# Performance work log

Measured on AMD Instinct MI355X. Metric: run time of the kernel, lower is better.

## Reference

```python
import jax, jax.numpy as jnp
import numpy as np

SR = 32000
N_FFT = 1024
HOP = 320
N_MELS = 128
PCEN_EPS = 1e-6
LN_EPS = 1e-6


def _hz_to_mel(f):
    return 2595.0 * np.log10(1.0 + f / 700.0)


def _mel_to_hz(m):
    return 700.0 * (10.0 ** (m / 2595.0) - 1.0)


def make_mel_fb():
    # HTK-scale triangular mel filterbank, [n_freqs, n_mels] (torchaudio default)
    n_freqs = N_FFT // 2 + 1
    mels = np.linspace(_hz_to_mel(0.0), _hz_to_mel(SR / 2.0), N_MELS + 2)
    f_pts = _mel_to_hz(mels)                       # [n_mels+2]
    all_freqs = np.linspace(0.0, SR / 2.0, n_freqs)
    f_diff = f_pts[1:] - f_pts[:-1]
    slopes = f_pts[None, :] - all_freqs[:, None]   # [n_freqs, n_mels+2]
    down = -slopes[:, :-2] / f_diff[:-1]
    up = slopes[:, 2:] / f_diff[1:]
    fb = np.maximum(0.0, np.minimum(down, up))
    return fb.astype(np.float32)


def setup_inputs() -> dict:
    key = jax.random.key(0)
    x = jax.random.normal(key, (16, 320000), dtype=jnp.float32)
    return {
        "x": x,
        "mel_fb": jnp.asarray(make_mel_fb()),
        "log_s": jnp.asarray(np.log(0.025), dtype=jnp.float32),
        "log_alpha": jnp.asarray(np.log(0.98), dtype=jnp.float32),
        "log_delta": jnp.asarray(np.log(2.0), dtype=jnp.float32),
        "log_r": jnp.asarray(np.log(0.5), dtype=jnp.float32),
    }


def reference(x, mel_fb, log_s, log_alpha, log_delta, log_r):
    B, T = x.shape
    pad = N_FFT // 2
    xp = jnp.pad(x, ((0, 0), (pad, pad)), mode="reflect")
    n_frames = 1 + (xp.shape[1] - N_FFT) // HOP           # = T//HOP + 1
    idx = jnp.arange(n_frames)[:, None] * HOP + jnp.arange(N_FFT)[None, :]
    frames = xp[:, idx]                                    # [B, F, N_FFT]
    # periodic Hann window (torch.hann_window default)
    win = 0.5 * (1.0 - jnp.cos(2.0 * jnp.pi * jnp.arange(N_FFT) / N_FFT))
    spec = jnp.fft.rfft(frames * win, axis=-1)             # [B, F, N_FFT//2+1]
    power = spec.real ** 2 + spec.imag ** 2                # power spectrogram
    E = jnp.einsum("bfk,km->bfm", power, mel_fb)           # [B, F, M] mel energies

    s = jnp.exp(log_s)
    alpha = jnp.exp(log_alpha)
    delta = jnp.exp(log_delta)
    r = jnp.exp(log_r)

    # Causal exponential smoother M(t) = (1-s) M(t-1) + s E(t), M init = first frame
    E_t = jnp.swapaxes(E, 0, 1)                            # [F, B, M]

    def step(m, e):
        m = (1.0 - s) * m + s * e
        return m, m

    _, M_t = jax.lax.scan(step, E_t[0], E_t)
    smooth = jnp.swapaxes(M_t, 0, 1)                       # [B, F, M]

    pcen = (E / (PCEN_EPS + smooth) ** alpha + delta) ** r - delta ** r

    # affine-free layer_norm over last dim (n_mels), eps=1e-6
    mu = jnp.mean(pcen, axis=-1, keepdims=True)
    var = jnp.var(pcen, axis=-1, keepdims=True)
    return (pcen - mu) / jnp.sqrt(var + LN_EPS)
```

## Files before the change

kernel.cpp:

```cpp
#include <hip/hip_runtime.h>
#include <math.h>

#define SRATE   32000
#define NFFT    1024
#define HOP     320
#define NBINS   513
#define NMELS   128
#define NFRAMES 1001
#define NB      16
#define TLEN    320000
#define PCEN_EPS 1e-6f
#define LN_EPS   1e-6f
#define MAXW     64

#define CL      16
#define NCHUNK  63

__device__ __forceinline__ int P(int i) { return i + (i >> 3); }
#define ZPAD 1152

__global__ __launch_bounds__(256) void k_prep(
    const float* __restrict__ fb, int* __restrict__ kmin, int* __restrict__ klen,
    float* __restrict__ wv, float* __restrict__ win, float2* __restrict__ twg)
{
    const int blk = blockIdx.x;
    const int tid = threadIdx.x;
    if (blk < NMELS) {
        const int m = blk;
        __shared__ int smin[4], smax[4];
        int lmin = 1 << 30, lmax = -1;
        for (int k = tid; k < NBINS; k += 256) {
            if (fb[k * NMELS + m] > 0.f) {
                if (k < lmin) lmin = k;
                if (k > lmax) lmax = k;
            }
        }
        #pragma unroll
        for (int off = 32; off; off >>= 1) {
            int om = __shfl_xor(lmin, off); if (om < lmin) lmin = om;
            int ox = __shfl_xor(lmax, off); if (ox > lmax) lmax = ox;
        }
        if ((tid & 63) == 0) { smin[tid >> 6] = lmin; smax[tid >> 6] = lmax; }
        __syncthreads();
        int k0 = min(min(smin[0], smin[1]), min(smin[2], smin[3]));
        int k1 = max(max(smax[0], smax[1]), max(smax[2], smax[3]));
        int L  = (k1 < 0) ? 0 : min(k1 - k0 + 1, MAXW);
        if (tid == 0) { kmin[m] = (k1 < 0) ? 0 : k0; klen[m] = L; }
        if (tid < L) wv[m * MAXW + tid] = fb[(k0 + tid) * NMELS + m];
    } else {
        const int i = (blk - NMELS) * 256 + tid;
        if (i < NFFT) {
            float sp = sinpif((float)i * (1.0f / (float)NFFT));
            win[i] = sp * sp;
        } else if (i < NFFT + 256) {
            int n = i - NFFT;
            float sn, cn;
            sincospif((float)n * (1.0f / 512.0f), &sn, &cn);
            twg[n] = make_float2(cn, -sn);
        }
    }
}

__global__ __launch_bounds__(256) void k_melspec(
    const float* __restrict__ x,
    const int*   __restrict__ kmin,
    const int*   __restrict__ klen,
    const float* __restrict__ wv,
    const float* __restrict__ fb,
    const float* __restrict__ win_g,
    const float2* __restrict__ twg,
    float* __restrict__ E,
    int usePacked)
{
    __shared__ float2 zA[ZPAD], zB[ZPAD];
    __shared__ float2 tws[256];

    const int tid = threadIdx.x;
    const int g   = blockIdx.x;
    const int f0  = 2 * g, f1 = 2 * g + 1;
    const int b0  = f0 / NFRAMES, t0f = f0 - b0 * NFRAMES;
    const int b1  = f1 / NFRAMES, t1f = f1 - b1 * NFRAMES;
    const float* xb0 = x + (size_t)b0 * TLEN;
    const float* xb1 = x + (size_t)b1 * TLEN;

    if (usePacked) {
        tws[tid] = twg[tid];
    } else {
        float sn, cn;
        sincospif((float)tid * (1.0f / 512.0f), &sn, &cn);
        tws[tid] = make_float2(cn, -sn);
    }

    const int base0 = t0f * HOP - (NFFT / 2);
    const int base1 = t1f * HOP - (NFFT / 2);
    const int i0 = tid * 4;
    const bool safe = usePacked &&
                      base0 >= 0 && base1 >= 0 &&
                      (base0 + NFFT - 1 < TLEN) && (base1 + NFFT - 1 < TLEN);
    if (safe) {
        float4 v0 = *(const float4*)(xb0 + base0 + i0);
        float4 v1 = *(const float4*)(xb1 + base1 + i0);
        float4 w  = *(const float4*)(win_g + i0);
        zA[P(i0 + 0)] = make_float2(v0.x * w.x, v1.x * w.x);
        zA[P(i0 + 1)] = make_float2(v0.y * w.y, v1.y * w.y);
        zA[P(i0 + 2)] = make_float2(v0.z * w.z, v1.z * w.z);
        zA[P(i0 + 3)] = make_float2(v0.w * w.w, v1.w * w.w);
    } else {
        #pragma unroll
        for (int u = 0; u < 4; ++u) {
            const int i = i0 + u;
            int j0 = base0 + i;
            j0 = (j0 < 0) ? -j0 : ((j0 >= TLEN) ? (2 * TLEN - 2 - j0) : j0);
            int j1 = base1 + i;
            j1 = (j1 < 0) ? -j1 : ((j1 >= TLEN) ? (2 * TLEN - 2 - j1) : j1);
            float w;
            if (usePacked) w = win_g[i];
            else { float sp = sinpif((float)i * (1.0f / (float)NFFT)); w = sp * sp; }
            zA[P(i)] = make_float2(xb0[j0] * w, xb1[j1] * w);
        }
    }
    __syncthreads();

    float2 *zs = zA, *zd = zB;
    #pragma unroll
    for (int st = 0; st < 5; ++st) {
        const int mm = 1 << (2 * st);
        const int n  = tid & ~(mm - 1);
        const int o  = (n << 2) | (tid & (mm - 1));
        float2 a0 = zs[P(tid)];
        float2 a1 = zs[P(tid + 256)];
        float2 a2 = zs[P(tid + 512)];
        float2 a3 = zs[P(tid + 768)];
        float2 w1 = tws[n];
        float c1 = w1.x, s1 = w1.y;
        float c2 = c1 * c1 - s1 * s1, s2 = 2.f * c1 * s1;
        float c3 = c1 * c2 - s1 * s2, s3 = c1 * s2 + s1 * c2;
        float t0r = a0.x + a2.x, t0i = a0.y + a2.y;
        float t1r = a0.x - a2.x, t1i = a0.y - a2.y;
        float t2r = a1.x + a3.x, t2i = a1.y + a3.y;
        float t3r = a1.y - a3.y, t3i = a3.x - a1.x;
        float y1r = t1r + t3r, y1i = t1i + t3i;
        float y2r = t0r - t2r, y2i = t0i - t2i;
        float y3r = t1r - t3r, y3i = t1i - t3i;
        zd[P(o)]          = make_float2(t0r + t2r,            t0i + t2i);
        zd[P(o + mm)]     = make_float2(y1r * c1 - y1i * s1,  y1r * s1 + y1i * c1);
        zd[P(o + 2 * mm)] = make_float2(y2r * c2 - y2i * s2,  y2r * s2 + y2i * c2);
        zd[P(o + 3 * mm)] = make_float2(y3r * c3 - y3i * s3,  y3r * s3 + y3i * c3);
        __syncthreads();
        float2* tp = zs; zs = zd; zd = tp;
    }

    for (int k = tid; k < NBINS; k += 256) {
        float2 Z  = zs[P(k)];
        const int kr = (NFFT - k) & (NFFT - 1);
        float2 Zr = zs[P(kr)];
        float x1r = Z.x + Zr.x, x1i = Z.y - Zr.y;
        float x2r = Z.y + Zr.y, x2i = Zr.x - Z.x;
        zd[P(k)] = make_float2(0.25f * (x1r * x1r + x1i * x1i),
                               0.25f * (x2r * x2r + x2i * x2i));
    }
    __syncthreads();

    if (tid < NMELS) {
        const int m = tid;
        float acc0 = 0.f, acc1 = 0.f;
        if (usePacked) {
            const int k0 = kmin[m], L = klen[m];
            const float* w = wv + m * MAXW;
            for (int j = 0; j < L; ++j) {
                float2 pk = zd[P(k0 + j)];
                float ww = w[j];
                acc0 += pk.x * ww; acc1 += pk.y * ww;
            }
        } else {
            for (int k = 0; k < NBINS; ++k) {
                float2 pk = zd[P(k)];
                float ww = fb[k * NMELS + m];
                acc0 += pk.x * ww; acc1 += pk.y * ww;
            }
        }
        E[(size_t)f0 * NMELS + m] = acc0;
        E[(size_t)f1 * NMELS + m] = acc1;
    }
}

__global__ __launch_bounds__(256) void k_pcen_chunk(
    const float* __restrict__ E, float* __restrict__ Bws,
    float* __restrict__ E0ws, const float* __restrict__ p_ls)
{
    const int gid = blockIdx.x * blockDim.x + threadIdx.x;
    const int m = gid & (NMELS - 1);
    const int c = (gid >> 7) % NCHUNK;
    const int b = gid / (NMELS * NCHUNK);

    const float s = expf(p_ls[0]);
    const float a = 1.f - s;

    const int t0 = c * CL;
    const int L  = (t0 + CL <= NFRAMES) ? CL : (NFRAMES - t0);
    const float* col = E + (size_t)b * NFRAMES * NMELS + m;

    if (c == 0) E0ws[b * NMELS + m] = col[0];

    float Bacc;
    if (L == CL) {
        float e[CL];
        #pragma unroll
        for (int j = 0; j < CL; ++j)
            e[j] = col[(size_t)(t0 + j) * NMELS];
        float p0 = 0.f, p1 = 0.f, p2 = 0.f, p3 = 0.f;
        #pragma unroll
        for (int u = 0; u < 4; ++u) {
            p0 = a * p0 + s * e[u];
            p1 = a * p1 + s * e[4 + u];
            p2 = a * p2 + s * e[8 + u];
            p3 = a * p3 + s * e[12 + u];
        }
        const float a2 = a * a, a4 = a2 * a2, a8 = a4 * a4, a12 = a8 * a4;
        Bacc = a12 * p0 + a8 * p1 + a4 * p2 + p3;
    } else {
        Bacc = 0.f;
        for (int j = 0; j < L; ++j)
            Bacc = a * Bacc + s * col[(size_t)(t0 + j) * NMELS];
    }
    Bws[gid] = Bacc;
}

__global__ __launch_bounds__(256) void k_pcen_ln(
    float* __restrict__ E, const float* __restrict__ Bws,
    const float* __restrict__ E0ws,
    const float* __restrict__ p_ls, const float* __restrict__ p_la,
    const float* __restrict__ p_ld, const float* __restrict__ p_lr)
{
    __shared__ float sm[2 * CL][NMELS];

    const int tid  = threadIdx.x;
    const int half = tid >> 7;
    const int m    = tid & 127;
    const int b    = blockIdx.x >> 5;
    const int cp   = blockIdx.x & 31;
    const int c    = cp * 2 + half;

    const float s     = expf(p_ls[0]);
    const float alpha = expf(p_la[0]);
    const float delta = expf(p_ld[0]);
    const float r     = expf(p_lr[0]);
    const float dr    = __powf(delta, r);
    const float a     = 1.f - s;
    const float a2 = a * a, a4 = a2 * a2, a8 = a4 * a4;
    const float a16 = a8 * a8;

    if (c < NCHUNK) {
        float M = E0ws[b * NMELS + m];
        const float* Bcol = Bws + (size_t)b * NCHUNK * NMELS + m;
        int cc = 0;
        for (; cc + 8 <= c; cc += 8) {
            float b0 = Bcol[(size_t)(cc + 0) * NMELS];
            float b1 = Bcol[(size_t)(cc + 1) * NMELS];
            float b2 = Bcol[(size_t)(cc + 2) * NMELS];
            float b3 = Bcol[(size_t)(cc + 3) * NMELS];
            float b4 = Bcol[(size_t)(cc + 4) * NMELS];
            float b5 = Bcol[(size_t)(cc + 5) * NMELS];
            float b6 = Bcol[(size_t)(cc + 6) * NMELS];
            float b7 = Bcol[(size_t)(cc + 7) * NMELS];
            M = a16 * M + b0; M = a16 * M + b1; M = a16 * M + b2; M = a16 * M + b3;
            M = a16 * M + b4; M = a16 * M + b5; M = a16 * M + b6; M = a16 * M + b7;
        }
        for (; cc < c; ++cc)
            M = a16 * M + Bcol[(size_t)cc * NMELS];

        const int t0 = c * CL;
        const int L  = (t0 + CL <= NFRAMES) ? CL : (NFRAMES - t0);
        const float* col = E + ((size_t)b * NFRAMES + t0) * NMELS + m;
        for (int j = 0; j < L; ++j) {
            float e = col[(size_t)j * NMELS];
            M = a * M + s * e;
            float den = __powf(PCEN_EPS + M, alpha);
            sm[half * CL + j][m] = __powf(e / den + delta, r) - dr;
        }
    }
    __syncthreads();

    const int wid  = tid >> 6;
    const int lane = tid & 63;
    for (int row = wid; row < 2 * CL; row += 4) {
        const int cc = cp * 2 + (row >> 4);
        if (cc >= NCHUNK) continue;
        const int j   = row & (CL - 1);
        const int tt0 = cc * CL;
        const int LL  = (tt0 + CL <= NFRAMES) ? CL : (NFRAMES - tt0);
        if (j >= LL) continue;
        float v0 = sm[row][lane], v1 = sm[row][lane + 64];
        float sum = v0 + v1;
        float sq  = v0 * v0 + v1 * v1;
        #pragma unroll
        for (int off = 32; off; off >>= 1) {
            sum += __shfl_xor(sum, off);
            sq  += __shfl_xor(sq,  off);
        }
        float mu  = sum * (1.f / 128.f);
        float var = sq * (1.f / 128.f) - mu * mu;
        float inv = rsqrtf(var + LN_EPS);
        float* p = E + ((size_t)b * NFRAMES + tt0 + j) * NMELS;
        p[lane]      = (v0 - mu) * inv;
        p[lane + 64] = (v1 - mu) * inv;
    }
}

__global__ __launch_bounds__(256) void k_pcen_serial(
    float* __restrict__ E,
    const float* __restrict__ p_ls, const float* __restrict__ p_la,
    const float* __restrict__ p_ld, const float* __restrict__ p_lr)
{
    const int gid = blockIdx.x * blockDim.x + threadIdx.x;
    const int b = gid >> 7;
    const int m = gid & 127;

    const float s     = expf(p_ls[0]);
    const float alpha = expf(p_la[0]);
    const float delta = expf(p_ld[0]);
    const float r     = expf(p_lr[0]);
    const float dr    = powf(delta, r);
    const float a     = 1.f - s;

    float* col = E + (size_t)b * NFRAMES * NMELS + m;
    float M = col[0];
    for (int t = 0; t < NFRAMES; ++t) {
        float e = col[(size_t)t * NMELS];
        M = a * M + s * e;
        float den = __powf(PCEN_EPS + M, alpha);
        float p   = __powf(e / den + delta, r) - dr;
        col[(size_t)t * NMELS] = p;
    }
}

__global__ __launch_bounds__(256) void k_ln(float* __restrict__ out) {
    const int wid  = threadIdx.x >> 6;
    const int lane = threadIdx.x & 63;
    const int row  = blockIdx.x * 4 + wid;
    float* p = out + (size_t)row * NMELS;
    float v0 = p[lane], v1 = p[lane + 64];
    float sum = v0 + v1;
    float sq  = v0 * v0 + v1 * v1;
    #pragma unroll
    for (int off = 32; off; off >>= 1) {
        sum += __shfl_xor(sum, off);
        sq  += __shfl_xor(sq,  off);
    }
    float mu  = sum * (1.f / 128.f);
    float var = sq * (1.f / 128.f) - mu * mu;
    float inv = rsqrtf(var + LN_EPS);
    p[lane]      = (v0 - mu) * inv;
    p[lane + 64] = (v1 - mu) * inv;
}

extern "C" void kernel_launch(void* const* d_in, const int* in_sizes, int n_in,
                              void* d_out, int out_size, void* d_ws, size_t ws_size,
                              hipStream_t stream) {
    const float* x   = (const float*)d_in[0];
    const float* fb  = (const float*)d_in[1];
    const float* lsp = (const float*)d_in[2];
    const float* lap = (const float*)d_in[3];
    const float* ldp = (const float*)d_in[4];
    const float* lrp = (const float*)d_in[5];
    float* out = (float*)d_out;

    const size_t packElems = 128 + 128 + 8192 + 1024 + 512;
    const size_t scanElems = (size_t)NB * NCHUNK * NMELS;
    const size_t needPack  = packElems * 4;
    const size_t needScan  = (packElems + scanElems + (size_t)NB * NMELS) * 4;

    int usePacked = (ws_size >= needPack) ? 1 : 0;
    int useScan   = (ws_size >= needScan) ? 1 : 0;

    int*    kmin = (int*)d_ws;
    int*    klen = kmin + NMELS;
    float*  wv   = (float*)(klen + NMELS);
    float*  win  = wv + (size_t)NMELS * MAXW;
    float2* twg  = (float2*)(win + NFFT);
    float*  Bws  = (float*)(twg + 256);
    float*  E0ws = Bws + scanElems;

    if (usePacked)
        k_prep<<<NMELS + 5, 256, 0, stream>>>(fb, kmin, klen, wv, win, twg);

    k_melspec<<<NB * NFRAMES / 2, 256, 0, stream>>>(
        x, kmin, klen, wv, fb, win, twg, out, usePacked);

    if (useScan) {
        const int nThread = NB * NCHUNK * NMELS;
        k_pcen_chunk<<<nThread / 256, 256, 0, stream>>>(out, Bws, E0ws, lsp);
        k_pcen_ln<<<NB * 32, 256, 0, stream>>>(out, Bws, E0ws, lsp, lap, ldp, lrp);
    } else {
        k_pcen_serial<<<(NB * NMELS) / 256, 256, 0, stream>>>(out, lsp, lap, ldp, lrp);
        k_ln<<<(NB * NFRAMES) / 4, 256, 0, stream>>>(out);
    }
}
```

Before: 75.80 us.

## Process four frames per melspec block and split pcen_ln into per-chunk blocks

The mel-spectrogram kernel now handles two packed complex FFTs (four frames) per 256-thread block. This spreads twiddle setup over more work and keeps all 256 threads busy in the mel projection, where only half were active before. The PCEN+LayerNorm kernel moves to one 128-thread block per chunk and fully unrolls the 16-frame loads into registers to expose memory-level parallelism. In exchange, melspec uses twice the shared memory per block and launches half as many blocks, which may reduce occupancy.

Result: slower. 77.69 us (+2.5%).

```diff
diff --git a/kernel.cpp b/kernel.cpp
--- a/kernel.cpp
+++ b/kernel.cpp
@@ -61,7 +61,7 @@
     }
 }
 
-__global__ __launch_bounds__(256) void k_melspec(
+__global__ __launch_bounds__(256, 4) void k_melspec(
     const float* __restrict__ x,
     const int*   __restrict__ kmin,
     const int*   __restrict__ klen,
@@ -72,16 +72,11 @@
     float* __restrict__ E,
     int usePacked)
 {
-    __shared__ float2 zA[ZPAD], zB[ZPAD];
+    __shared__ float2 zA[2][ZPAD], zB[2][ZPAD];
     __shared__ float2 tws[256];
 
     const int tid = threadIdx.x;
     const int g   = blockIdx.x;
-    const int f0  = 2 * g, f1 = 2 * g + 1;
-    const int b0  = f0 / NFRAMES, t0f = f0 - b0 * NFRAMES;
-    const int b1  = f1 / NFRAMES, t1f = f1 - b1 * NFRAMES;
-    const float* xb0 = x + (size_t)b0 * TLEN;
-    const float* xb1 = x + (size_t)b1 * TLEN;
 
     if (usePacked) {
         tws[tid] = twg[tid];
@@ -91,96 +86,115 @@
         tws[tid] = make_float2(cn, -sn);
     }
 
-    const int base0 = t0f * HOP - (NFFT / 2);
-    const int base1 = t1f * HOP - (NFFT / 2);
     const int i0 = tid * 4;
-    const bool safe = usePacked &&
-                      base0 >= 0 && base1 >= 0 &&
-                      (base0 + NFFT - 1 < TLEN) && (base1 + NFFT - 1 < TLEN);
-    if (safe) {
-        float4 v0 = *(const float4*)(xb0 + base0 + i0);
-        float4 v1 = *(const float4*)(xb1 + base1 + i0);
-        float4 w  = *(const float4*)(win_g + i0);
-        zA[P(i0 + 0)] = make_float2(v0.x * w.x, v1.x * w.x);
-        zA[P(i0 + 1)] = make_float2(v0.y * w.y, v1.y * w.y);
-        zA[P(i0 + 2)] = make_float2(v0.z * w.z, v1.z * w.z);
-        zA[P(i0 + 3)] = make_float2(v0.w * w.w, v1.w * w.w);
-    } else {
-        #pragma unroll
-        for (int u = 0; u < 4; ++u) {
-            const int i = i0 + u;
-            int j0 = base0 + i;
-            j0 = (j0 < 0) ? -j0 : ((j0 >= TLEN) ? (2 * TLEN - 2 - j0) : j0);
-            int j1 = base1 + i;
-            j1 = (j1 < 0) ? -j1 : ((j1 >= TLEN) ? (2 * TLEN - 2 - j1) : j1);
-            float w;
-            if (usePacked) w = win_g[i];
-            else { float sp = sinpif((float)i * (1.0f / (float)NFFT)); w = sp * sp; }
-            zA[P(i)] = make_float2(xb0[j0] * w, xb1[j1] * w);
+    #pragma unroll
+    for (int u = 0; u < 2; ++u) {
+        const int fa = 4 * g + 2 * u;
+        const int fbr = fa + 1;
+        const int ba = fa / NFRAMES,  ta = fa  - ba * NFRAMES;
+        const int bb = fbr / NFRAMES, tb = fbr - bb * NFRAMES;
+        const float* xa = x + (size_t)ba * TLEN;
+        const float* xb = x + (size_t)bb * TLEN;
+        const int basea = ta * HOP - (NFFT / 2);
+        const int baseb = tb * HOP - (NFFT / 2);
+        const bool safe = usePacked &&
+                          basea >= 0 && baseb >= 0 &&
+                          (basea + NFFT - 1 < TLEN) && (baseb + NFFT - 1 < TLEN);
+        if (safe) {
+            float4 v0 = *(const float4*)(xa + basea + i0);
+            float4 v1 = *(const float4*)(xb + baseb + i0);
+            float4 w  = *(const float4*)(win_g + i0);
+            zA[u][P(i0 + 0)] = make_float2(v0.x * w.x, v1.x * w.x);
+            zA[u][P(i0 + 1)] = make_float2(v0.y * w.y, v1.y * w.y);
+            zA[u][P(i0 + 2)] = make_float2(v0.z * w.z, v1.z * w.z);
+            zA[u][P(i0 + 3)] = make_float2(v0.w * w.w, v1.w * w.w);
+        } else {
+            #pragma unroll
+            for (int q = 0; q < 4; ++q) {
+                const int i = i0 + q;
+                int j0 = basea + i;
+                j0 = (j0 < 0) ? -j0 : ((j0 >= TLEN) ? (2 * TLEN - 2 - j0) : j0);
+                int j1 = baseb + i;
+                j1 = (j1 < 0) ? -j1 : ((j1 >= TLEN) ? (2 * TLEN - 2 - j1) : j1);
+                float w;
+                if (usePacked) w = win_g[i];
+                else { float sp = sinpif((float)i * (1.0f / (float)NFFT)); w = sp * sp; }
+                zA[u][P(i)] = make_float2(xa[j0] * w, xb[j1] * w);
+            }
         }
     }
     __syncthreads();
 
-    float2 *zs = zA, *zd = zB;
+    float2 (*zs)[ZPAD] = zA;
+    float2 (*zd)[ZPAD] = zB;
     #pragma unroll
     for (int st = 0; st < 5; ++st) {
         const int mm = 1 << (2 * st);
         const int n  = tid & ~(mm - 1);
         const int o  = (n << 2) | (tid & (mm - 1));
-        float2 a0 = zs[P(tid)];
-        float2 a1 = zs[P(tid + 256)];
-        float2 a2 = zs[P(tid + 512)];
-        float2 a3 = zs[P(tid + 768)];
         float2 w1 = tws[n];
-        float c1 = w1.x, s1 = w1.y;
-        float c2 = c1 * c1 - s1 * s1, s2 = 2.f * c1 * s1;
-        float c3 = c1 * c2 - s1 * s2, s3 = c1 * s2 + s1 * c2;
-        float t0r = a0.x + a2.x, t0i = a0.y + a2.y;
-        float t1r = a0.x - a2.x, t1i = a0.y - a2.y;
-        float t2r = a1.x + a3.x, t2i = a1.y + a3.y;
-        float t3r = a1.y - a3.y, t3i = a3.x - a1.x;
-        float y1r = t1r + t3r, y1i = t1i + t3i;
-        float y2r = t0r - t2r, y2i = t0i - t2i;
-        float y3r = t1r - t3r, y3i = t1i - t3i;
-        zd[P(o)]          = make_float2(t0r + t2r,            t0i + t2i);
-        zd[P(o + mm)]     = make_float2(y1r * c1 - y1i * s1,  y1r * s1 + y1i * c1);
-        zd[P(o + 2 * mm)] = make_float2(y2r * c2 - y2i * s2,  y2r * s2 + y2i * c2);
-        zd[P(o + 3 * mm)] = make_float2(y3r * c3 - y3i * s3,  y3r * s3 + y3i * c3);
+        const float c1 = w1.x, s1 = w1.y;
+        const float c2 = c1 * c1 - s1 * s1, s2 = 2.f * c1 * s1;
+        const float c3 = c1 * c2 - s1 * s2, s3 = c1 * s2 + s1 * c2;
+        #pragma unroll
+        for (int u = 0; u < 2; ++u) {
+            float2 a0 = zs[u][P(tid)];
+            float2 a1 = zs[u][P(tid + 256)];
+            float2 a2 = zs[u][P(tid + 512)];
+            float2 a3 = zs[u][P(tid + 768)];
+            float t0r = a0.x + a2.x, t0i = a0.y + a2.y;
+            float t1r = a0.x - a2.x, t1i = a0.y - a2.y;
+            float t2r = a1.x + a3.x, t2i = a1.y + a3.y;
+            float t3r = a1.y - a3.y, t3i = a3.x - a1.x;
+            float y1r = t1r + t3r, y1i = t1i + t3i;
+            float y2r = t0r - t2r, y2i = t0i - t2i;
+            float y3r = t1r - t3r, y3i = t1i - t3i;
+            zd[u][P(o)]          = make_float2(t0r + t2r,            t0i + t2i);
+            zd[u][P(o + mm)]     = make_float2(y1r * c1 - y1i * s1,  y1r * s1 + y1i * c1);
+            zd[u][P(o + 2 * mm)] = make_float2(y2r * c2 - y2i * s2,  y2r * s2 + y2i * c2);
+            zd[u][P(o + 3 * mm)] = make_float2(y3r * c3 - y3i * s3,  y3r * s3 + y3i * c3);
+        }
         __syncthreads();
-        float2* tp = zs; zs = zd; zd = tp;
-    }
-
-    for (int k = tid; k < NBINS; k += 256) {
-        float2 Z  = zs[P(k)];
-        const int kr = (NFFT - k) & (NFFT - 1);
-        float2 Zr = zs[P(kr)];
-        float x1r = Z.x + Zr.x, x1i = Z.y - Zr.y;
-        float x2r = Z.y + Zr.y, x2i = Zr.x - Z.x;
-        zd[P(k)] = make_float2(0.25f * (x1r * x1r + x1i * x1i),
-                               0.25f * (x2r * x2r + x2i * x2i));
+        float2 (*tp)[ZPAD] = zs; zs = zd; zd = tp;
+    }
+
+    {
+        const int u  = tid >> 7;
+        const int kk = tid & 127;
+        for (int k = kk; k < NBINS; k += 128) {
+            float2 Z  = zs[u][P(k)];
+            const int kr = (NFFT - k) & (NFFT - 1);
+            float2 Zr = zs[u][P(kr)];
+            float x1r = Z.x + Zr.x, x1i = Z.y - Zr.y;
+            float x2r = Z.y + Zr.y, x2i = Zr.x - Z.x;
+            zd[u][P(k)] = make_float2(0.25f * (x1r * x1r + x1i * x1i),
+                                      0.25f * (x2r * x2r + x2i * x2i));
+        }
     }
     __syncthreads();
 
-    if (tid < NMELS) {
-        const int m = tid;
+    {
+        const int u = tid >> 7;
+        const int m = tid & 127;
+        const int fa = 4 * g + 2 * u;
         float acc0 = 0.f, acc1 = 0.f;
         if (usePacked) {
             const int k0 = kmin[m], L = klen[m];
             const float* w = wv + m * MAXW;
             for (int j = 0; j < L; ++j) {
-                float2 pk = zd[P(k0 + j)];
+                float2 pk = zd[u][P(k0 + j)];
                 float ww = w[j];
                 acc0 += pk.x * ww; acc1 += pk.y * ww;
             }
         } else {
             for (int k = 0; k < NBINS; ++k) {
-                float2 pk = zd[P(k)];
+                float2 pk = zd[u][P(k)];
                 float ww = fb[k * NMELS + m];
                 acc0 += pk.x * ww; acc1 += pk.y * ww;
             }
         }
-        E[(size_t)f0 * NMELS + m] = acc0;
-        E[(size_t)f1 * NMELS + m] = acc1;
+        E[(size_t)fa * NMELS + m]       = acc0;
+        E[(size_t)(fa + 1) * NMELS + m] = acc1;
     }
 }
 
@@ -226,20 +240,18 @@
     Bws[gid] = Bacc;
 }
 
-__global__ __launch_bounds__(256) void k_pcen_ln(
+__global__ __launch_bounds__(128) void k_pcen_ln(
     float* __restrict__ E, const float* __restrict__ Bws,
     const float* __restrict__ E0ws,
     const float* __restrict__ p_ls, const float* __restrict__ p_la,
     const float* __restrict__ p_ld, const float* __restrict__ p_lr)
 {
-    __shared__ float sm[2 * CL][NMELS];
-
-    const int tid  = threadIdx.x;
-    const int half = tid >> 7;
-    const int m    = tid & 127;
-    const int b    = blockIdx.x >> 5;
-    const int cp   = blockIdx.x & 31;
-    const int c    = cp * 2 + half;
+    __shared__ float sm[CL][NMELS];
+
+    const int m   = threadIdx.x;
+    const int blk = blockIdx.x;
+    const int b   = blk / NCHUNK;
+    const int c   = blk - b * NCHUNK;
 
     const float s     = expf(p_ls[0]);
     const float alpha = expf(p_la[0]);
@@ -250,46 +262,52 @@
     const float a2 = a * a, a4 = a2 * a2, a8 = a4 * a4;
     const float a16 = a8 * a8;
 
-    if (c < NCHUNK) {
-        float M = E0ws[b * NMELS + m];
-        const float* Bcol = Bws + (size_t)b * NCHUNK * NMELS + m;
-        int cc = 0;
-        for (; cc + 8 <= c; cc += 8) {
-            float b0 = Bcol[(size_t)(cc + 0) * NMELS];
-            float b1 = Bcol[(size_t)(cc + 1) * NMELS];
-            float b2 = Bcol[(size_t)(cc + 2) * NMELS];
-            float b3 = Bcol[(size_t)(cc + 3) * NMELS];
-            float b4 = Bcol[(size_t)(cc + 4) * NMELS];
-            float b5 = Bcol[(size_t)(cc + 5) * NMELS];
-            float b6 = Bcol[(size_t)(cc + 6) * NMELS];
-            float b7 = Bcol[(size_t)(cc + 7) * NMELS];
-            M = a16 * M + b0; M = a16 * M + b1; M = a16 * M + b2; M = a16 * M + b3;
-            M = a16 * M + b4; M = a16 * M + b5; M = a16 * M + b6; M = a16 * M + b7;
-        }
-        for (; cc < c; ++cc)
-            M = a16 * M + Bcol[(size_t)cc * NMELS];
-
-        const int t0 = c * CL;
-        const int L  = (t0 + CL <= NFRAMES) ? CL : (NFRAMES - t0);
-        const float* col = E + ((size_t)b * NFRAMES + t0) * NMELS + m;
+    float M = E0ws[b * NMELS + m];
+    const float* Bcol = Bws + (size_t)b * NCHUNK * NMELS + m;
+    int cc = 0;
+    for (; cc + 8 <= c; cc += 8) {
+        float b0 = Bcol[(size_t)(cc + 0) * NMELS];
+        float b1 = Bcol[(size_t)(cc + 1) * NMELS];
+        float b2 = Bcol[(size_t)(cc + 2) * NMELS];
+        float b3 = Bcol[(size_t)(cc + 3) * NMELS];
+        float b4 = Bcol[(size_t)(cc + 4) * NMELS];
+        float b5 = Bcol[(size_t)(cc + 5) * NMELS];
+        float b6 = Bcol[(size_t)(cc + 6) * NMELS];
+        float b7 = Bcol[(size_t)(cc + 7) * NMELS];
+        M = a16 * M + b0; M = a16 * M + b1; M = a16 * M + b2; M = a16 * M + b3;
+        M = a16 * M + b4; M = a16 * M + b5; M = a16 * M + b6; M = a16 * M + b7;
+    }
+    for (; cc < c; ++cc)
+        M = a16 * M + Bcol[(size_t)cc * NMELS];
+
+    const int t0 = c * CL;
+    const int L  = (t0 + CL <= NFRAMES) ? CL : (NFRAMES - t0);
+    const float* col = E + ((size_t)b * NFRAMES + t0) * NMELS + m;
+
+    if (L == CL) {
+        float e[CL];
+        #pragma unroll
+        for (int j = 0; j < CL; ++j)
+            e[j] = col[(size_t)j * NMELS];
+        #pragma unroll
+        for (int j = 0; j < CL; ++j) {
+            M = a * M + s * e[j];
+            float den = __powf(PCEN_EPS + M, alpha);
+            sm[j][m] = __powf(e[j] / den + delta, r) - dr;
+        }
+    } else {
         for (int j = 0; j < L; ++j) {
             float e = col[(size_t)j * NMELS];
             M = a * M + s * e;
             float den = __powf(PCEN_EPS + M, alpha);
-            sm[half * CL + j][m] = __powf(e / den + delta, r) - dr;
+            sm[j][m] = __powf(e / den + delta, r) - dr;
         }
     }
     __syncthreads();
 
-    const int wid  = tid >> 6;
-    const int lane = tid & 63;
-    for (int row = wid; row < 2 * CL; row += 4) {
-        const int cc = cp * 2 + (row >> 4);
-        if (cc >= NCHUNK) continue;
-        const int j   = row & (CL - 1);
-        const int tt0 = cc * CL;
-        const int LL  = (tt0 + CL <= NFRAMES) ? CL : (NFRAMES - tt0);
-        if (j >= LL) continue;
+    const int wid  = m >> 6;
+    const int lane = m & 63;
+    for (int row = wid; row < L; row += 2) {
         float v0 = sm[row][lane], v1 = sm[row][lane + 64];
         float sum = v0 + v1;
         float sq  = v0 * v0 + v1 * v1;
@@ -301,7 +319,7 @@
         float mu  = sum * (1.f / 128.f);
         float var = sq * (1.f / 128.f) - mu * mu;
         float inv = rsqrtf(var + LN_EPS);
-        float* p = E + ((size_t)b * NFRAMES + tt0 + j) * NMELS;
+        float* p = E + ((size_t)b * NFRAMES + t0 + row) * NMELS;
         p[lane]      = (v0 - mu) * inv;
         p[lane + 64] = (v1 - mu) * inv;
     }
@@ -384,13 +402,13 @@
     if (usePacked)
         k_prep<<<NMELS + 5, 256, 0, stream>>>(fb, kmin, klen, wv, win, twg);
 
-    k_melspec<<<NB * NFRAMES / 2, 256, 0, stream>>>(
+    k_melspec<<<NB * NFRAMES / 4, 256, 0, stream>>>(
         x, kmin, klen, wv, fb, win, twg, out, usePacked);
 
     if (useScan) {
         const int nThread = NB * NCHUNK * NMELS;
         k_pcen_chunk<<<nThread / 256, 256, 0, stream>>>(out, Bws, E0ws, lsp);
-        k_pcen_ln<<<NB * 32, 256, 0, stream>>>(out, Bws, E0ws, lsp, lap, ldp, lrp);
+        k_pcen_ln<<<NB * NCHUNK, 128, 0, stream>>>(out, Bws, E0ws, lsp, lap, ldp, lrp);
     } else {
         k_pcen_serial<<<(NB * NMELS) / 256, 256, 0, stream>>>(out, lsp, lap, ldp, lrp);
         k_ln<<<(NB * NFRAMES) / 4, 256, 0, stream>>>(out);
```

## Replace shared-memory radix-4 FFT with register 32x32 four-step FFT

Applied to the files above, without the earlier changes.

The 1024-point FFT moves from five shared-memory radix-4 stages with a barrier after each to a four-step 32x32 decomposition. Each thread runs an in-register radix-2 FFT over 32 points, with one twiddle pass and a single shared-memory transpose in between. Each block now handles 8 frames (4 packed complex pairs) instead of 2, and the real-split power step is fused into the mel accumulation. This cuts barriers and LDS traffic, but only 128 of 256 threads do FFT work and register pressure from the 32-element complex arrays is high. Global loads are strided by 32 rather than vectorised float4.

Result: slower. 93.94 us (+23.9%).

```diff
diff --git a/kernel.cpp b/kernel.cpp
--- a/kernel.cpp
+++ b/kernel.cpp
@@ -16,12 +16,44 @@
 #define CL      16
 #define NCHUNK  63
 
-__device__ __forceinline__ int P(int i) { return i + (i >> 3); }
-#define ZPAD 1152
+#define CPF     4
+#define LPITCH  33
+
+__device__ __constant__ static const int BR5_[1] = {0};
+constexpr int BR5[32] = {0,16,8,24,4,20,12,28,2,18,10,26,6,22,14,30,
+                         1,17,9,25,5,21,13,29,3,19,11,27,7,23,15,31};
+
+__device__ __forceinline__ void fft32(float2* y) {
+    constexpr float C16[16] = {
+        1.f, 0.98078528f, 0.92387953f, 0.83146961f,
+        0.70710678f, 0.55557023f, 0.38268343f, 0.19509032f,
+        0.f, -0.19509032f, -0.38268343f, -0.55557023f,
+        -0.70710678f, -0.83146961f, -0.92387953f, -0.98078528f};
+    constexpr float S16[16] = {
+        0.f, 0.19509032f, 0.38268343f, 0.55557023f,
+        0.70710678f, 0.83146961f, 0.92387953f, 0.98078528f,
+        1.f, 0.98078528f, 0.92387953f, 0.83146961f,
+        0.70710678f, 0.55557023f, 0.38268343f, 0.19509032f};
+    #pragma unroll
+    for (int h = 16; h >= 1; h >>= 1) {
+        #pragma unroll
+        for (int b = 0; b < 32; b += 2 * h) {
+            #pragma unroll
+            for (int j = 0; j < h; ++j) {
+                float2 u = y[b + j], w = y[b + j + h];
+                float sr = u.x - w.x, si = u.y - w.y;
+                y[b + j] = make_float2(u.x + w.x, u.y + w.y);
+                const float wr = C16[j * (16 / h)];
+                const float wi = -S16[j * (16 / h)];
+                y[b + j + h] = make_float2(sr * wr - si * wi, sr * wi + si * wr);
+            }
+        }
+    }
+}
 
 __global__ __launch_bounds__(256) void k_prep(
     const float* __restrict__ fb, int* __restrict__ kmin, int* __restrict__ klen,
-    float* __restrict__ wv, float* __restrict__ win, float2* __restrict__ twg)
+    float* __restrict__ wv, float* __restrict__ winT, float2* __restrict__ twrow)
 {
     const int blk = blockIdx.x;
     const int tid = threadIdx.x;
@@ -51,12 +83,14 @@
         const int i = (blk - NMELS) * 256 + tid;
         if (i < NFFT) {
             float sp = sinpif((float)i * (1.0f / (float)NFFT));
-            win[i] = sp * sp;
-        } else if (i < NFFT + 256) {
-            int n = i - NFFT;
+            winT[((i & 31) << 5) | (i >> 5)] = sp * sp;
+        } else {
+            const int e = i - NFFT;
+            const int c = e >> 5, k1 = e & 31;
+            const int n = c * k1;
             float sn, cn;
             sincospif((float)n * (1.0f / 512.0f), &sn, &cn);
-            twg[n] = make_float2(cn, -sn);
+            twrow[e] = make_float2(cn, -sn);
         }
     }
 }
@@ -67,120 +101,117 @@
     const int*   __restrict__ klen,
     const float* __restrict__ wv,
     const float* __restrict__ fb,
-    const float* __restrict__ win_g,
-    const float2* __restrict__ twg,
+    const float* __restrict__ winT,
+    const float2* __restrict__ twrow,
     float* __restrict__ E,
     int usePacked)
 {
-    __shared__ float2 zA[ZPAD], zB[ZPAD];
-    __shared__ float2 tws[256];
+    __shared__ float2 Ld[CPF][LPITCH * 32];
 
     const int tid = threadIdx.x;
     const int g   = blockIdx.x;
-    const int f0  = 2 * g, f1 = 2 * g + 1;
-    const int b0  = f0 / NFRAMES, t0f = f0 - b0 * NFRAMES;
-    const int b1  = f1 / NFRAMES, t1f = f1 - b1 * NFRAMES;
-    const float* xb0 = x + (size_t)b0 * TLEN;
-    const float* xb1 = x + (size_t)b1 * TLEN;
-
-    if (usePacked) {
-        tws[tid] = twg[tid];
-    } else {
-        float sn, cn;
-        sincospif((float)tid * (1.0f / 512.0f), &sn, &cn);
-        tws[tid] = make_float2(cn, -sn);
-    }
-
-    const int base0 = t0f * HOP - (NFFT / 2);
-    const int base1 = t1f * HOP - (NFFT / 2);
-    const int i0 = tid * 4;
-    const bool safe = usePacked &&
-                      base0 >= 0 && base1 >= 0 &&
-                      (base0 + NFFT - 1 < TLEN) && (base1 + NFFT - 1 < TLEN);
-    if (safe) {
-        float4 v0 = *(const float4*)(xb0 + base0 + i0);
-        float4 v1 = *(const float4*)(xb1 + base1 + i0);
-        float4 w  = *(const float4*)(win_g + i0);
-        zA[P(i0 + 0)] = make_float2(v0.x * w.x, v1.x * w.x);
-        zA[P(i0 + 1)] = make_float2(v0.y * w.y, v1.y * w.y);
-        zA[P(i0 + 2)] = make_float2(v0.z * w.z, v1.z * w.z);
-        zA[P(i0 + 3)] = make_float2(v0.w * w.w, v1.w * w.w);
-    } else {
-        #pragma unroll
-        for (int u = 0; u < 4; ++u) {
-            const int i = i0 + u;
-            int j0 = base0 + i;
-            j0 = (j0 < 0) ? -j0 : ((j0 >= TLEN) ? (2 * TLEN - 2 - j0) : j0);
-            int j1 = base1 + i;
-            j1 = (j1 < 0) ? -j1 : ((j1 >= TLEN) ? (2 * TLEN - 2 - j1) : j1);
-            float w;
-            if (usePacked) w = win_g[i];
-            else { float sp = sinpif((float)i * (1.0f / (float)NFFT)); w = sp * sp; }
-            zA[P(i)] = make_float2(xb0[j0] * w, xb1[j1] * w);
+
+    if (tid < 32 * CPF) {
+        const int v = tid >> 5, c = tid & 31;
+        const int fa = 8 * g + 2 * v, fbf = fa + 1;
+        const int ba = fa / NFRAMES,  ta = fa  - ba * NFRAMES;
+        const int bb = fbf / NFRAMES, tb = fbf - bb * NFRAMES;
+        const float* xa = x + (size_t)ba * TLEN;
+        const float* xb = x + (size_t)bb * TLEN;
+        const int basea = ta * HOP - (NFFT / 2);
+        const int baseb = tb * HOP - (NFFT / 2);
+        float2 y[32];
+        const bool safe = (basea >= 0) && (baseb >= 0) &&
+                          (basea + NFFT - 1 < TLEN) && (baseb + NFFT - 1 < TLEN);
+        if (usePacked && safe) {
+            #pragma unroll
+            for (int r = 0; r < 32; ++r) {
+                const int i = c + 32 * r;
+                const float w = winT[(c << 5) + r];
+                y[r] = make_float2(xa[basea + i] * w, xb[baseb + i] * w);
+            }
+        } else {
+            #pragma unroll
+            for (int r = 0; r < 32; ++r) {
+                const int i = c + 32 * r;
+                int ja = basea + i;
+                ja = (ja < 0) ? -ja : ((ja >= TLEN) ? (2 * TLEN - 2 - ja) : ja);
+                int jb = baseb + i;
+                jb = (jb < 0) ? -jb : ((jb >= TLEN) ? (2 * TLEN - 2 - jb) : jb);
+                float w;
+                if (usePacked) w = winT[(c << 5) + r];
+                else { float sp = sinpif((float)i * (1.0f / (float)NFFT)); w = sp * sp; }
+                y[r] = make_float2(xa[ja] * w, xb[jb] * w);
+            }
+        }
+        fft32(y);
+        const float2* trow = twrow + (c << 5);
+        #pragma unroll
+        for (int k1 = 0; k1 < 32; ++k1) {
+            float2 val = y[BR5[k1]];
+            float2 w;
+            if (usePacked) w = trow[k1];
+            else {
+                float sn, cn;
+                sincospif((float)(c * k1) * (1.0f / 512.0f), &sn, &cn);
+                w = make_float2(cn, -sn);
+            }
+            Ld[v][LPITCH * c + k1] =
+                make_float2(val.x * w.x - val.y * w.y,
+                            val.x * w.y + val.y * w.x);
         }
     }
     __syncthreads();
 
-    float2 *zs = zA, *zd = zB;
-    #pragma unroll
-    for (int st = 0; st < 5; ++st) {
-        const int mm = 1 << (2 * st);
-        const int n  = tid & ~(mm - 1);
-        const int o  = (n << 2) | (tid & (mm - 1));
-        float2 a0 = zs[P(tid)];
-        float2 a1 = zs[P(tid + 256)];
-        float2 a2 = zs[P(tid + 512)];
-        float2 a3 = zs[P(tid + 768)];
-        float2 w1 = tws[n];
-        float c1 = w1.x, s1 = w1.y;
-        float c2 = c1 * c1 - s1 * s1, s2 = 2.f * c1 * s1;
-        float c3 = c1 * c2 - s1 * s2, s3 = c1 * s2 + s1 * c2;
-        float t0r = a0.x + a2.x, t0i = a0.y + a2.y;
-        float t1r = a0.x - a2.x, t1i = a0.y - a2.y;
-        float t2r = a1.x + a3.x, t2i = a1.y + a3.y;
-        float t3r = a1.y - a3.y, t3i = a3.x - a1.x;
-        float y1r = t1r + t3r, y1i = t1i + t3i;
-        float y2r = t0r - t2r, y2i = t0i - t2i;
-        float y3r = t1r - t3r, y3i = t1i - t3i;
-        zd[P(o)]          = make_float2(t0r + t2r,            t0i + t2i);
-        zd[P(o + mm)]     = make_float2(y1r * c1 - y1i * s1,  y1r * s1 + y1i * c1);
-        zd[P(o + 2 * mm)] = make_float2(y2r * c2 - y2i * s2,  y2r * s2 + y2i * c2);
-        zd[P(o + 3 * mm)] = make_float2(y3r * c3 - y3i * s3,  y3r * s3 + y3i * c3);
-        __syncthreads();
-        float2* tp = zs; zs = zd; zd = tp;
-    }
-
-    for (int k = tid; k < NBINS; k += 256) {
-        float2 Z  = zs[P(k)];
-        const int kr = (NFFT - k) & (NFFT - 1);
-        float2 Zr = zs[P(kr)];
-        float x1r = Z.x + Zr.x, x1i = Z.y - Zr.y;
-        float x2r = Z.y + Zr.y, x2i = Zr.x - Z.x;
-        zd[P(k)] = make_float2(0.25f * (x1r * x1r + x1i * x1i),
-                               0.25f * (x2r * x2r + x2i * x2i));
+    if (tid < 32 * CPF) {
+        const int v = tid >> 5, k1 = tid & 31;
+        float2 y[32];
+        #pragma unroll
+        for (int cc = 0; cc < 32; ++cc) y[cc] = Ld[v][LPITCH * cc + k1];
+        fft32(y);
+        #pragma unroll
+        for (int k2 = 0; k2 < 32; ++k2)
+            Ld[v][LPITCH * k2 + k1] = y[BR5[k2]];
     }
     __syncthreads();
 
-    if (tid < NMELS) {
-        const int m = tid;
-        float acc0 = 0.f, acc1 = 0.f;
-        if (usePacked) {
-            const int k0 = kmin[m], L = klen[m];
-            const float* w = wv + m * MAXW;
-            for (int j = 0; j < L; ++j) {
-                float2 pk = zd[P(k0 + j)];
-                float ww = w[j];
-                acc0 += pk.x * ww; acc1 += pk.y * ww;
-            }
-        } else {
-            for (int k = 0; k < NBINS; ++k) {
-                float2 pk = zd[P(k)];
-                float ww = fb[k * NMELS + m];
-                acc0 += pk.x * ww; acc1 += pk.y * ww;
-            }
-        }
-        E[(size_t)f0 * NMELS + m] = acc0;
-        E[(size_t)f1 * NMELS + m] = acc1;
+    {
+        const int m  = tid & 127;
+        const int vh = tid >> 7;
+        #pragma unroll
+        for (int q = 0; q < 2; ++q) {
+            const int vv = vh + 2 * q;
+            const int f0 = 8 * g + 2 * vv;
+            float acc0 = 0.f, acc1 = 0.f;
+            if (usePacked) {
+                const int k0 = kmin[m], L = klen[m];
+                const float* w = wv + m * MAXW;
+                for (int j = 0; j < L; ++j) {
+                    const int k  = k0 + j;
+                    const int kr = (NFFT - k) & (NFFT - 1);
+                    float2 Z  = Ld[vv][LPITCH * (k  >> 5) + (k  & 31)];
+                    float2 Zr = Ld[vv][LPITCH * (kr >> 5) + (kr & 31)];
+                    float x1r = Z.x + Zr.x, x1i = Z.y - Zr.y;
+                    float x2r = Z.y + Zr.y, x2i = Zr.x - Z.x;
+                    float ww = w[j];
+                    acc0 += (x1r * x1r + x1i * x1i) * ww;
+                    acc1 += (x2r * x2r + x2i * x2i) * ww;
+                }
+            } else {
+                for (int k = 0; k < NBINS; ++k) {
+                    const int kr = (NFFT - k) & (NFFT - 1);
+                    float2 Z  = Ld[vv][LPITCH * (k  >> 5) + (k  & 31)];
+                    float2 Zr = Ld[vv][LPITCH * (kr >> 5) + (kr & 31)];
+                    float x1r = Z.x + Zr.x, x1i = Z.y - Zr.y;
+                    float x2r = Z.y + Zr.y, x2i = Zr.x - Z.x;
+                    float ww = fb[k * NMELS + m];
+                    acc0 += (x1r * x1r + x1i * x1i) * ww;
+                    acc1 += (x2r * x2r + x2i * x2i) * ww;
+                }
+            }
+            E[(size_t)f0 * NMELS + m]       = 0.25f * acc0;
+            E[(size_t)(f0 + 1) * NMELS + m] = 0.25f * acc1;
+        }
     }
 }
 
@@ -365,7 +396,7 @@
     const float* lrp = (const float*)d_in[5];
     float* out = (float*)d_out;
 
-    const size_t packElems = 128 + 128 + 8192 + 1024 + 512;
+    const size_t packElems = 128 + 128 + 8192 + 1024 + 2048;
     const size_t scanElems = (size_t)NB * NCHUNK * NMELS;
     const size_t needPack  = packElems * 4;
     const size_t needScan  = (packElems + scanElems + (size_t)NB * NMELS) * 4;
@@ -373,19 +404,19 @@
     int usePacked = (ws_size >= needPack) ? 1 : 0;
     int useScan   = (ws_size >= needScan) ? 1 : 0;
 
-    int*    kmin = (int*)d_ws;
-    int*    klen = kmin + NMELS;
-    float*  wv   = (float*)(klen + NMELS);
-    float*  win  = wv + (size_t)NMELS * MAXW;
-    float2* twg  = (float2*)(win + NFFT);
-    float*  Bws  = (float*)(twg + 256);
-    float*  E0ws = Bws + scanElems;
+    int*    kmin  = (int*)d_ws;
+    int*    klen  = kmin + NMELS;
+    float*  wv    = (float*)(klen + NMELS);
+    float*  winT  = wv + (size_t)NMELS * MAXW;
+    float2* twrow = (float2*)(winT + NFFT);
+    float*  Bws   = (float*)(twrow + 1024);
+    float*  E0ws  = Bws + scanElems;
 
     if (usePacked)
-        k_prep<<<NMELS + 5, 256, 0, stream>>>(fb, kmin, klen, wv, win, twg);
-
-    k_melspec<<<NB * NFRAMES / 2, 256, 0, stream>>>(
-        x, kmin, klen, wv, fb, win, twg, out, usePacked);
+        k_prep<<<NMELS + 8, 256, 0, stream>>>(fb, kmin, klen, wv, winT, twrow);
+
+    k_melspec<<<NB * NFRAMES / 8, 256, 0, stream>>>(
+        x, kmin, klen, wv, fb, winT, twrow, out, usePacked);
 
     if (useScan) {
         const int nThread = NB * NCHUNK * NMELS;
```
